# Kernel tuning notes

Measured on AMD Instinct MI355X. Metric: run time of the kernel, lower is better.

## Reference

```python
import jax, jax.numpy as jnp
import numpy as np

B, S, D, H = 4, 1024, 1024, 16
DH = D // H  # head_dim = 64


def setup_inputs() -> dict:
    key = jax.random.key(0)
    kq, kk, kv, kl, kwq, kwk, kwv, kwo = jax.random.split(key, 8)
    query = jax.random.normal(kq, (B, S, D), dtype=jnp.float32)
    key_t = jax.random.normal(kk, (B, S, D), dtype=jnp.float32)
    value = jax.random.normal(kv, (B, S, D), dtype=jnp.float32)
    # padding: keys at positions >= valid length are padded (True)
    lengths = jax.random.randint(kl, (B,), S // 2, S + 1)
    key_padding_mask = jnp.arange(S)[None, :] >= lengths[:, None]  # [B,S] bool
    scale = 1.0 / np.sqrt(D)
    Wq = jax.random.normal(kwq, (D, D), dtype=jnp.float32) * scale
    Wk = jax.random.normal(kwk, (D, D), dtype=jnp.float32) * scale
    Wv = jax.random.normal(kwv, (D, D), dtype=jnp.float32) * scale
    Wo = jax.random.normal(kwo, (D, D), dtype=jnp.float32) * scale
    gamma = jnp.ones((H,), dtype=jnp.float32)
    return {"query": query, "key": key_t, "value": value,
            "key_padding_mask": key_padding_mask,
            "Wq": Wq, "Wk": Wk, "Wv": Wv, "Wo": Wo, "gamma": gamma}


def reference(query, key, value, key_padding_mask, Wq, Wk, Wv, Wo, gamma):
    # nn.Linear(x) = x @ W.T (bias=False)
    q = jnp.einsum('bsd,ed->bse', query, Wq).reshape(B, S, H, DH).transpose(0, 2, 1, 3)  # [B,H,S,Dh]
    k = jnp.einsum('bsd,ed->bse', key, Wk).reshape(B, S, H, DH).transpose(0, 2, 1, 3)
    v = jnp.einsum('bsd,ed->bse', value, Wv).reshape(B, S, H, DH).transpose(0, 2, 1, 3)
    scores = jnp.einsum('bhqd,bhkd->bhqk', q, k) / jnp.sqrt(jnp.float32(DH))
    pad = key_padding_mask[:, None, None, :]  # [B,1,1,S]
    scores = jnp.where(pad, -jnp.inf, scores)
    v = jnp.where(key_padding_mask[:, None, :, None], 0.0, v)
    attn = jax.nn.softmax(scores, axis=-1)  # dropout p=0 (eval) -> identity
    ws = jnp.einsum('bhqk,bhkd->bhqd', attn, v)
    ws = ws * gamma[None, :, None, None]  # per-head scale
    ws = ws.transpose(0, 2, 1, 3).reshape(B, S, D)
    return jnp.einsum('bsd,ed->bse', ws, Wo)
```

## Files before the change

### kernel.cpp

```cpp
#include <hip/hip_runtime.h>
#include <math.h>

typedef __attribute__((ext_vector_type(8))) short bf16x8;
typedef __attribute__((ext_vector_type(4))) short bf16x4;
typedef __attribute__((ext_vector_type(4))) float f32x4;

#define MFMA16(a, b, c) __builtin_amdgcn_mfma_f32_16x16x32_bf16(a, b, c, 0, 0, 0)

#define WPL (1024u * 1024u)
#define XPL (4u * 1024u * 1024u)

__device__ __forceinline__ unsigned short rne_bf16(float f) {
    unsigned u = __float_as_uint(f);
    u += 0x7FFFu + ((u >> 16) & 1u);
    return (unsigned short)(u >> 16);
}

typedef const __attribute__((address_space(1))) unsigned int* gas_t;
typedef __attribute__((address_space(3))) unsigned int* las_t;
__device__ __forceinline__ void glds16(const void* g, void* l) {
    __builtin_amdgcn_global_load_lds((gas_t)g, (las_t)l, 16, 0, 0);
}

__global__ __launch_bounds__(256)
void convert_all(const float* __restrict__ Wq, const float* __restrict__ Wk,
                 const float* __restrict__ Wv, const float* __restrict__ Wo,
                 const float* __restrict__ Xq, const float* __restrict__ Xk,
                 const float* __restrict__ Xv,
                 unsigned short* __restrict__ Wb, unsigned short* __restrict__ Xb) {
    int blk = blockIdx.x;
    const float* S;
    unsigned short* D;
    if (blk < 4096) {
        int which = blk >> 10;
        S = which == 0 ? Wq : which == 1 ? Wk : which == 2 ? Wv : Wo;
        D = Wb + (size_t)which * WPL;
        blk &= 1023;
    } else {
        blk -= 4096;
        int which = blk >> 12;
        S = which == 0 ? Xq : which == 1 ? Xk : Xv;
        D = Xb + (size_t)which * XPL;
        blk &= 4095;
    }
    int i = (blk * 256 + threadIdx.x) * 4;
    float4 f = *(const float4*)&S[i];
    bf16x4 h;
    h[0] = (short)rne_bf16(f.x);
    h[1] = (short)rne_bf16(f.y);
    h[2] = (short)rne_bf16(f.z);
    h[3] = (short)rne_bf16(f.w);
    *(bf16x4*)&D[i] = h;
}

__global__ __launch_bounds__(256)
void gemm_ab(const unsigned short* __restrict__ Abase,
             const unsigned short* __restrict__ Bbase,
             unsigned short* __restrict__ QKV, float* __restrict__ Cf,
             int modeBase) {
    __shared__ unsigned short AS[128 * 64], BS[128 * 64];
    const int z = blockIdx.z, mode = modeBase + z;
    const unsigned short* A = Abase + (size_t)z * XPL;
    const unsigned short* B = Bbase + (size_t)z * WPL;

    const int t = threadIdx.x, lane = t & 63, w = t >> 6;
    const int quad = lane >> 4, l15 = lane & 15;
    const int wr = w & 1, wc = w >> 1;
    const int rowBase = blockIdx.y * 128, colBase = blockIdx.x * 128;

    const int srow = lane >> 3;
    const int cg = ((lane & 7) + 2 * srow) & 7;
    const unsigned short *gA[4], *gB[4];
    unsigned short *lA[4], *lB[4];
    #pragma unroll
    for (int e = 0; e < 4; e++) {
        int row = e * 32 + w * 8 + srow;
        gA[e] = A + (size_t)(rowBase + row) * 1024 + cg * 8;
        gB[e] = B + (size_t)(colBase + row) * 1024 + cg * 8;
        lA[e] = &AS[(e * 32 + w * 8) * 64];
        lB[e] = &BS[(e * 32 + w * 8) * 64];
    }

    const int s0 = (quad - 2 * l15) & 7;
    const int c0 = s0 * 8, c1 = ((s0 + 4) & 7) * 8;
    int aOff[4], bOff[4];
    #pragma unroll
    for (int i = 0; i < 4; i++) {
        aOff[i] = (wr * 64 + i * 16 + l15) * 64;
        bOff[i] = (wc * 64 + i * 16 + l15) * 64;
    }

    f32x4 acc[4][4] = {};

    for (int kt = 0; kt < 16; kt++) {
        if (kt) __syncthreads();
        const int ko = kt * 64;
        #pragma unroll
        for (int e = 0; e < 4; e++) {
            glds16(gA[e] + ko, lA[e]);
            glds16(gB[e] + ko, lB[e]);
        }
        __syncthreads();

        bf16x8 af[4], bfr[4];
        #pragma unroll
        for (int i = 0; i < 4; i++) af[i] = *(const bf16x8*)&AS[aOff[i] + c0];
        #pragma unroll
        for (int j = 0; j < 4; j++) bfr[j] = *(const bf16x8*)&BS[bOff[j] + c0];
        #pragma unroll
        for (int j = 0; j < 4; j++)
            #pragma unroll
            for (int i = 0; i < 4; i++)
                acc[i][j] = MFMA16(af[i], bfr[j], acc[i][j]);

        #pragma unroll
        for (int i = 0; i < 4; i++) af[i] = *(const bf16x8*)&AS[aOff[i] + c1];
        #pragma unroll
        for (int j = 0; j < 4; j++) bfr[j] = *(const bf16x8*)&BS[bOff[j] + c1];
        #pragma unroll
        for (int j = 0; j < 4; j++)
            #pragma unroll
            for (int i = 0; i < 4; i++)
                acc[i][j] = MFMA16(af[i], bfr[j], acc[i][j]);
    }

    if (mode == 3) {
        #pragma unroll
        for (int i = 0; i < 4; i++)
            #pragma unroll
            for (int j = 0; j < 4; j++)
                #pragma unroll
                for (int r = 0; r < 4; r++) {
                    int m = rowBase + wr * 64 + i * 16 + quad * 4 + r;
                    int n = colBase + wc * 64 + j * 16 + l15;
                    Cf[(size_t)m * 1024 + n] = acc[i][j][r];
                }
    } else {
        unsigned short* O = QKV + (size_t)z * XPL;
        #pragma unroll
        for (int i = 0; i < 4; i++)
            #pragma unroll
            for (int j = 0; j < 4; j++)
                #pragma unroll
                for (int r = 0; r < 4; r++) {
                    int m = rowBase + wr * 64 + i * 16 + quad * 4 + r;
                    int n = colBase + wc * 64 + j * 16 + l15;
                    int bb = m >> 10, s = m & 1023, hh = n >> 6, dh = n & 63;
                    size_t hb = ((size_t)(bb * 16 + hh)) << 16;
                    unsigned short v = rne_bf16(acc[i][j][r]);
                    if (mode == 0) {
                        O[hb + s * 64 + dh] = v;
                    } else if (mode == 1) {
                        O[hb + (size_t)((s >> 4) * 2 + (dh >> 5)) * 512 +
                          ((dh >> 3) & 3) * 128 + (s & 15) * 8 + (dh & 7)] = v;
                    } else {
                        O[hb + (size_t)((dh >> 4) * 32 + (s >> 5)) * 512 +
                          ((s >> 3) & 3) * 128 + (dh & 15) * 8 + (s & 7)] = v;
                    }
                }
    }
}

__global__ __launch_bounds__(256)
void attn_flat(const unsigned short* __restrict__ Qp,
               const unsigned short* __restrict__ Kf,
               const unsigned short* __restrict__ Vf,
               const int* __restrict__ mask, const float* __restrict__ gamma,
               unsigned short* __restrict__ WSr) {
    __shared__ int maskS[1024];
    __shared__ unsigned short Ph[4][32 * 72];

    const int t = threadIdx.x, lane = t & 63, w = t >> 6;
    const int quad = lane >> 4, l15 = lane & 15;
    const int q0 = blockIdx.x * 128, h = blockIdx.y, b = blockIdx.z;
    const size_t hb = ((size_t)(b * 16 + h)) << 16;

    ((int4*)maskS)[t] = ((const int4*)(mask + b * 1024))[t];

    bf16x8 qf[2][2];
    #pragma unroll
    for (int mi = 0; mi < 2; mi++) {
        size_t qb = hb + (size_t)(q0 + w * 32 + mi * 16 + l15) * 64 + quad * 8;
        qf[mi][0] = *(const bf16x8*)&Qp[qb];
        qf[mi][1] = *(const bf16x8*)&Qp[qb + 32];
    }

    f32x4 o[2][4] = {};
    float lsum[2][4] = {{0.f, 0.f, 0.f, 0.f}, {0.f, 0.f, 0.f, 0.f}};
    unsigned short* P = Ph[w];

    __syncthreads();

    for (int jt = 0; jt < 16; jt++) {
        const int j0 = jt * 64;
        if (maskS[j0]) break;
        const bool partial = maskS[j0 + 63] != 0;

        bf16x8 kv[4][2];
        #pragma unroll
        for (int nj = 0; nj < 4; nj++)
            #pragma unroll
            for (int kk = 0; kk < 2; kk++)
                kv[nj][kk] = *(const bf16x8*)&Kf[hb + (size_t)((jt * 4 + nj) * 2 + kk) * 512 + lane * 8];

        f32x4 s4[2][4] = {};
        #pragma unroll
        for (int nj = 0; nj < 4; nj++)
            #pragma unroll
            for (int kk = 0; kk < 2; kk++)
                #pragma unroll
                for (int mi = 0; mi < 2; mi++)
                    s4[mi][nj] = MFMA16(qf[mi][kk], kv[nj][kk], s4[mi][nj]);

        bf16x8 vv[4][2];
        #pragma unroll
        for (int dt = 0; dt < 4; dt++)
            #pragma unroll
            for (int ks = 0; ks < 2; ks++)
                vv[dt][ks] = *(const bf16x8*)&Vf[hb + (size_t)(dt * 32 + jt * 2 + ks) * 512 + lane * 8];

        #pragma unroll
        for (int mi = 0; mi < 2; mi++)
            #pragma unroll
            for (int nj = 0; nj < 4; nj++) {
                int mk = partial ? maskS[j0 + nj * 16 + l15] : 0;
                #pragma unroll
                for (int r = 0; r < 4; r++) {
                    float p = mk ? 0.f : __expf(s4[mi][nj][r] * 0.125f);
                    lsum[mi][r] += p;
                    int rowW = mi * 16 + quad * 4 + r;
                    int slot = ((nj * 2 + (l15 >> 3)) - 2 * rowW) & 7;
                    P[rowW * 72 + slot * 8 + (l15 & 7)] = rne_bf16(p);
                }
            }

        bf16x8 pf[2][2];
        #pragma unroll
        for (int mi = 0; mi < 2; mi++) {
            int rowR = mi * 16 + l15;
            int sl0 = (quad - 2 * rowR) & 7;
            pf[mi][0] = *(const bf16x8*)&P[rowR * 72 + sl0 * 8];
            pf[mi][1] = *(const bf16x8*)&P[rowR * 72 + ((sl0 + 4) & 7) * 8];
        }
        #pragma unroll
        for (int dt = 0; dt < 4; dt++)
            #pragma unroll
            for (int ks = 0; ks < 2; ks++)
                #pragma unroll
                for (int mi = 0; mi < 2; mi++)
                    o[mi][dt] = MFMA16(pf[mi][ks], vv[dt][ks], o[mi][dt]);
    }

    #pragma unroll
    for (int mi = 0; mi < 2; mi++)
        #pragma unroll
        for (int r = 0; r < 4; r++) {
            lsum[mi][r] += __shfl_xor(lsum[mi][r], 1);
            lsum[mi][r] += __shfl_xor(lsum[mi][r], 2);
            lsum[mi][r] += __shfl_xor(lsum[mi][r], 4);
            lsum[mi][r] += __shfl_xor(lsum[mi][r], 8);
        }

    const float g = gamma[h];
    #pragma unroll
    for (int mi = 0; mi < 2; mi++)
        #pragma unroll
        for (int r = 0; r < 4; r++) {
            int qrow = q0 + w * 32 + mi * 16 + quad * 4 + r;
            float sc = g / lsum[mi][r];
            size_t base = ((size_t)b * 1024 + qrow) * 1024 + h * 64;
            #pragma unroll
            for (int dt = 0; dt < 4; dt++)
                WSr[base + dt * 16 + l15] = rne_bf16(o[mi][dt][r] * sc);
        }
}

extern "C" void kernel_launch(void* const* d_in, const int* in_sizes, int n_in,
                              void* d_out, int out_size, void* d_ws, size_t ws_size,
                              hipStream_t stream) {
    const float* query = (const float*)d_in[0];
    const float* key   = (const float*)d_in[1];
    const float* value = (const float*)d_in[2];
    const int*   mask  = (const int*)d_in[3];
    const float* Wq    = (const float*)d_in[4];
    const float* Wk    = (const float*)d_in[5];
    const float* Wv    = (const float*)d_in[6];
    const float* Wo    = (const float*)d_in[7];
    const float* gamma = (const float*)d_in[8];
    float* out = (float*)d_out;

    unsigned short* u = (unsigned short*)d_ws;
    unsigned short* Xb  = u;
    unsigned short* QKV = u + 3 * XPL;
    unsigned short* Wb  = u + 6 * XPL;
    unsigned short* WSr = Xb;
    unsigned short* Qp = QKV, *Kfp = QKV + XPL, *Vfp = QKV + 2 * XPL;
    unsigned short* Wob = Wb + 3 * WPL;

    convert_all<<<16384, 256, 0, stream>>>(Wq, Wk, Wv, Wo, query, key, value, Wb, Xb);

    gemm_ab<<<dim3(8, 32, 3), 256, 0, stream>>>(Xb, Wb, QKV, nullptr, 0);

    attn_flat<<<dim3(8, 16, 4), 256, 0, stream>>>(Qp, Kfp, Vfp, mask, gamma, WSr);

    gemm_ab<<<dim3(8, 32, 1), 256, 0, stream>>>(WSr, Wob, nullptr, out, 3);
}
```

Before: 217.1 us.

## Double-buffer LDS tiles in GEMM to prefetch next K-slice during MFMA

Splits the shared-memory A/B tiles into two buffers. The next K tile is issued via global_load_lds into the alternate buffer before computing on the current one, with a single barrier per iteration. The aim is to overlap global-to-LDS transfer latency with MFMA compute. In exchange, LDS use per block doubles, which may lower occupancy, and correctness relies on the barrier waiting for outstanding async LDS loads.

```diff
diff --git a/kernel.cpp b/kernel.cpp
--- a/kernel.cpp
+++ b/kernel.cpp
@@ -58,7 +58,7 @@
              const unsigned short* __restrict__ Bbase,
              unsigned short* __restrict__ QKV, float* __restrict__ Cf,
              int modeBase) {
-    __shared__ unsigned short AS[128 * 64], BS[128 * 64];
+    __shared__ unsigned short AS[2][128 * 64], BS[2][128 * 64];
     const int z = blockIdx.z, mode = modeBase + z;
     const unsigned short* A = Abase + (size_t)z * XPL;
     const unsigned short* B = Bbase + (size_t)z * WPL;
@@ -71,14 +71,13 @@
     const int srow = lane >> 3;
     const int cg = ((lane & 7) + 2 * srow) & 7;
     const unsigned short *gA[4], *gB[4];
-    unsigned short *lA[4], *lB[4];
+    int lOff[4];
     #pragma unroll
     for (int e = 0; e < 4; e++) {
         int row = e * 32 + w * 8 + srow;
         gA[e] = A + (size_t)(rowBase + row) * 1024 + cg * 8;
         gB[e] = B + (size_t)(colBase + row) * 1024 + cg * 8;
-        lA[e] = &AS[(e * 32 + w * 8) * 64];
-        lB[e] = &BS[(e * 32 + w * 8) * 64];
+        lOff[e] = (e * 32 + w * 8) * 64;
     }
 
     const int s0 = (quad - 2 * l15) & 7;
@@ -92,21 +91,29 @@
 
     f32x4 acc[4][4] = {};
 
+    #pragma unroll
+    for (int e = 0; e < 4; e++) {
+        glds16(gA[e], &AS[0][lOff[e]]);
+        glds16(gB[e], &BS[0][lOff[e]]);
+    }
+    __syncthreads();
+
     for (int kt = 0; kt < 16; kt++) {
-        if (kt) __syncthreads();
-        const int ko = kt * 64;
-        #pragma unroll
-        for (int e = 0; e < 4; e++) {
-            glds16(gA[e] + ko, lA[e]);
-            glds16(gB[e] + ko, lB[e]);
+        const int buf = kt & 1;
+        if (kt + 1 < 16) {
+            const int ko = (kt + 1) * 64, nb = buf ^ 1;
+            #pragma unroll
+            for (int e = 0; e < 4; e++) {
+                glds16(gA[e] + ko, &AS[nb][lOff[e]]);
+                glds16(gB[e] + ko, &BS[nb][lOff[e]]);
+            }
         }
-        __syncthreads();
 
         bf16x8 af[4], bfr[4];
         #pragma unroll
-        for (int i = 0; i < 4; i++) af[i] = *(const bf16x8*)&AS[aOff[i] + c0];
-        #pragma unroll
-        for (int j = 0; j < 4; j++) bfr[j] = *(const bf16x8*)&BS[bOff[j] + c0];
+        for (int i = 0; i < 4; i++) af[i] = *(const bf16x8*)&AS[buf][aOff[i] + c0];
+        #pragma unroll
+        for (int j = 0; j < 4; j++) bfr[j] = *(const bf16x8*)&BS[buf][bOff[j] + c0];
         #pragma unroll
         for (int j = 0; j < 4; j++)
             #pragma unroll
@@ -114,14 +121,16 @@
                 acc[i][j] = MFMA16(af[i], bfr[j], acc[i][j]);
 
         #pragma unroll
-        for (int i = 0; i < 4; i++) af[i] = *(const bf16x8*)&AS[aOff[i] + c1];
-        #pragma unroll
-        for (int j = 0; j < 4; j++) bfr[j] = *(const bf16x8*)&BS[bOff[j] + c1];
+        for (int i = 0; i < 4; i++) af[i] = *(const bf16x8*)&AS[buf][aOff[i] + c1];
+        #pragma unroll
+        for (int j = 0; j < 4; j++) bfr[j] = *(const bf16x8*)&BS[buf][bOff[j] + c1];
         #pragma unroll
         for (int j = 0; j < 4; j++)
             #pragma unroll
             for (int i = 0; i < 4; i++)
                 acc[i][j] = MFMA16(af[i], bfr[j], acc[i][j]);
+
+        __syncthreads();
     }
 
     if (mode == 3) {
```

Measured after the change: 222.2 us. 1.02x slower.

## Split GEMM kernel, use BK=32 XOR-swizzled tiles and narrower output-projection tiles

Applied to the files above, without the earlier changes.

Replaces the shared mode-switched GEMM with two specialised kernels. The K tile shrinks from 64 to 32, which halves LDS use per block, and the shared-memory layout switches to an XOR swizzle. The output projection now uses 128x64 tiles, doubling its grid from 256 to 512 blocks so more CUs are busy. The cost is twice as many K iterations, each with its own barriers, and less MFMA work between syncs.

```diff
diff --git a/kernel.cpp b/kernel.cpp
--- a/kernel.cpp
+++ b/kernel.cpp
@@ -54,111 +54,165 @@
 }
 
 __global__ __launch_bounds__(256)
-void gemm_ab(const unsigned short* __restrict__ Abase,
-             const unsigned short* __restrict__ Bbase,
-             unsigned short* __restrict__ QKV, float* __restrict__ Cf,
-             int modeBase) {
-    __shared__ unsigned short AS[128 * 64], BS[128 * 64];
-    const int z = blockIdx.z, mode = modeBase + z;
-    const unsigned short* A = Abase + (size_t)z * XPL;
-    const unsigned short* B = Bbase + (size_t)z * WPL;
+void gemm_proj(const unsigned short* __restrict__ Xbase,
+               const unsigned short* __restrict__ Wb,
+               unsigned short* __restrict__ QKV) {
+    __shared__ unsigned short AS[128 * 32];
+    __shared__ unsigned short BS[128 * 32];
+
+    const int z = blockIdx.z;
+    const unsigned short* A = Xbase + (size_t)z * XPL;
+    const unsigned short* B = Wb + (size_t)z * WPL;
 
     const int t = threadIdx.x, lane = t & 63, w = t >> 6;
     const int quad = lane >> 4, l15 = lane & 15;
     const int wr = w & 1, wc = w >> 1;
     const int rowBase = blockIdx.y * 128, colBase = blockIdx.x * 128;
 
-    const int srow = lane >> 3;
-    const int cg = ((lane & 7) + 2 * srow) & 7;
-    const unsigned short *gA[4], *gB[4];
-    unsigned short *lA[4], *lB[4];
-    #pragma unroll
-    for (int e = 0; e < 4; e++) {
-        int row = e * 32 + w * 8 + srow;
+    const unsigned short* gA[2];
+    const unsigned short* gB[2];
+    unsigned short* lA[2];
+    unsigned short* lB[2];
+    #pragma unroll
+    for (int e = 0; e < 2; e++) {
+        int row = w * 32 + e * 16 + (lane >> 2);
+        int cg = (lane & 3) ^ ((row >> 1) & 3);
         gA[e] = A + (size_t)(rowBase + row) * 1024 + cg * 8;
         gB[e] = B + (size_t)(colBase + row) * 1024 + cg * 8;
-        lA[e] = &AS[(e * 32 + w * 8) * 64];
-        lB[e] = &BS[(e * 32 + w * 8) * 64];
-    }
-
-    const int s0 = (quad - 2 * l15) & 7;
-    const int c0 = s0 * 8, c1 = ((s0 + 4) & 7) * 8;
-    int aOff[4], bOff[4];
+        lA[e] = &AS[(w * 32 + e * 16) * 32];
+        lB[e] = &BS[(w * 32 + e * 16) * 32];
+    }
+
+    int aAd[4], bAd[4];
     #pragma unroll
     for (int i = 0; i < 4; i++) {
-        aOff[i] = (wr * 64 + i * 16 + l15) * 64;
-        bOff[i] = (wc * 64 + i * 16 + l15) * 64;
+        int ra = wr * 64 + i * 16 + l15;
+        aAd[i] = ra * 32 + (quad ^ ((ra >> 1) & 3)) * 8;
+        int rb = wc * 64 + i * 16 + l15;
+        bAd[i] = rb * 32 + (quad ^ ((rb >> 1) & 3)) * 8;
     }
 
     f32x4 acc[4][4] = {};
 
-    for (int kt = 0; kt < 16; kt++) {
+    for (int kt = 0; kt < 32; kt++) {
         if (kt) __syncthreads();
-        const int ko = kt * 64;
-        #pragma unroll
-        for (int e = 0; e < 4; e++) {
-            glds16(gA[e] + ko, lA[e]);
-            glds16(gB[e] + ko, lB[e]);
-        }
+        const int ko = kt * 32;
+        glds16(gA[0] + ko, lA[0]);
+        glds16(gA[1] + ko, lA[1]);
+        glds16(gB[0] + ko, lB[0]);
+        glds16(gB[1] + ko, lB[1]);
         __syncthreads();
 
         bf16x8 af[4], bfr[4];
         #pragma unroll
-        for (int i = 0; i < 4; i++) af[i] = *(const bf16x8*)&AS[aOff[i] + c0];
-        #pragma unroll
-        for (int j = 0; j < 4; j++) bfr[j] = *(const bf16x8*)&BS[bOff[j] + c0];
+        for (int i = 0; i < 4; i++) af[i] = *(const bf16x8*)&AS[aAd[i]];
+        #pragma unroll
+        for (int j = 0; j < 4; j++) bfr[j] = *(const bf16x8*)&BS[bAd[j]];
         #pragma unroll
         for (int j = 0; j < 4; j++)
             #pragma unroll
             for (int i = 0; i < 4; i++)
                 acc[i][j] = MFMA16(af[i], bfr[j], acc[i][j]);
-
-        #pragma unroll
-        for (int i = 0; i < 4; i++) af[i] = *(const bf16x8*)&AS[aOff[i] + c1];
-        #pragma unroll
-        for (int j = 0; j < 4; j++) bfr[j] = *(const bf16x8*)&BS[bOff[j] + c1];
+    }
+
+    unsigned short* O = QKV + (size_t)z * XPL;
+    #pragma unroll
+    for (int i = 0; i < 4; i++)
         #pragma unroll
         for (int j = 0; j < 4; j++)
             #pragma unroll
+            for (int r = 0; r < 4; r++) {
+                int m = rowBase + wr * 64 + i * 16 + quad * 4 + r;
+                int n = colBase + wc * 64 + j * 16 + l15;
+                int bb = m >> 10, s = m & 1023, hh = n >> 6, dh = n & 63;
+                size_t hb = ((size_t)(bb * 16 + hh)) << 16;
+                unsigned short v = rne_bf16(acc[i][j][r]);
+                if (z == 0) {
+                    O[hb + s * 64 + dh] = v;
+                } else if (z == 1) {
+                    O[hb + (size_t)((s >> 4) * 2 + (dh >> 5)) * 512 +
+                      ((dh >> 3) & 3) * 128 + (s & 15) * 8 + (dh & 7)] = v;
+                } else {
+                    O[hb + (size_t)((dh >> 4) * 32 + (s >> 5)) * 512 +
+                      ((s >> 3) & 3) * 128 + (dh & 15) * 8 + (s & 7)] = v;
+                }
+            }
+}
+
+__global__ __launch_bounds__(256)
+void gemm_out1(const unsigned short* __restrict__ A,
+               const unsigned short* __restrict__ Bh,
+               float* __restrict__ Cf) {
+    __shared__ unsigned short AS[128 * 32];
+    __shared__ unsigned short BhS[64 * 32];
+
+    const int t = threadIdx.x, lane = t & 63, w = t >> 6;
+    const int quad = lane >> 4, l15 = lane & 15;
+    const int wr = w & 1, wc = w >> 1;
+    const int rowBase = blockIdx.y * 128, colBase = blockIdx.x * 64;
+
+    const unsigned short* gA[2];
+    unsigned short* lA[2];
+    #pragma unroll
+    for (int e = 0; e < 2; e++) {
+        int row = w * 32 + e * 16 + (lane >> 2);
+        int cg = (lane & 3) ^ ((row >> 1) & 3);
+        gA[e] = A + (size_t)(rowBase + row) * 1024 + cg * 8;
+        lA[e] = &AS[(w * 32 + e * 16) * 32];
+    }
+    const unsigned short* gBh;
+    unsigned short* lBh;
+    {
+        int row = w * 16 + (lane >> 2);
+        int cg = (lane & 3) ^ ((row >> 1) & 3);
+        gBh = Bh + (size_t)(colBase + row) * 1024 + cg * 8;
+        lBh = &BhS[(w * 16) * 32];
+    }
+
+    int aAd[4], bAd[2];
+    #pragma unroll
+    for (int i = 0; i < 4; i++) {
+        int ra = wr * 64 + i * 16 + l15;
+        aAd[i] = ra * 32 + (quad ^ ((ra >> 1) & 3)) * 8;
+    }
+    #pragma unroll
+    for (int j = 0; j < 2; j++) {
+        int rb = wc * 32 + j * 16 + l15;
+        bAd[j] = rb * 32 + (quad ^ ((rb >> 1) & 3)) * 8;
+    }
+
+    f32x4 acc[4][2] = {};
+
+    for (int kt = 0; kt < 32; kt++) {
+        if (kt) __syncthreads();
+        const int ko = kt * 32;
+        glds16(gA[0] + ko, lA[0]);
+        glds16(gA[1] + ko, lA[1]);
+        glds16(gBh + ko, lBh);
+        __syncthreads();
+
+        bf16x8 af[4], bhf[2];
+        #pragma unroll
+        for (int i = 0; i < 4; i++) af[i] = *(const bf16x8*)&AS[aAd[i]];
+        #pragma unroll
+        for (int j = 0; j < 2; j++) bhf[j] = *(const bf16x8*)&BhS[bAd[j]];
+        #pragma unroll
+        for (int j = 0; j < 2; j++)
+            #pragma unroll
             for (int i = 0; i < 4; i++)
-                acc[i][j] = MFMA16(af[i], bfr[j], acc[i][j]);
-    }
-
-    if (mode == 3) {
-        #pragma unroll
-        for (int i = 0; i < 4; i++)
-            #pragma unroll
-            for (int j = 0; j < 4; j++)
-                #pragma unroll
-                for (int r = 0; r < 4; r++) {
-                    int m = rowBase + wr * 64 + i * 16 + quad * 4 + r;
-                    int n = colBase + wc * 64 + j * 16 + l15;
-                    Cf[(size_t)m * 1024 + n] = acc[i][j][r];
-                }
-    } else {
-        unsigned short* O = QKV + (size_t)z * XPL;
-        #pragma unroll
-        for (int i = 0; i < 4; i++)
-            #pragma unroll
-            for (int j = 0; j < 4; j++)
-                #pragma unroll
-                for (int r = 0; r < 4; r++) {
-                    int m = rowBase + wr * 64 + i * 16 + quad * 4 + r;
-                    int n = colBase + wc * 64 + j * 16 + l15;
-                    int bb = m >> 10, s = m & 1023, hh = n >> 6, dh = n & 63;
-                    size_t hb = ((size_t)(bb * 16 + hh)) << 16;
-                    unsigned short v = rne_bf16(acc[i][j][r]);
-                    if (mode == 0) {
-                        O[hb + s * 64 + dh] = v;
-                    } else if (mode == 1) {
-                        O[hb + (size_t)((s >> 4) * 2 + (dh >> 5)) * 512 +
-                          ((dh >> 3) & 3) * 128 + (s & 15) * 8 + (dh & 7)] = v;
-                    } else {
-                        O[hb + (size_t)((dh >> 4) * 32 + (s >> 5)) * 512 +
-                          ((s >> 3) & 3) * 128 + (dh & 15) * 8 + (s & 7)] = v;
-                    }
-                }
-    }
+                acc[i][j] = MFMA16(af[i], bhf[j], acc[i][j]);
+    }
+
+    #pragma unroll
+    for (int i = 0; i < 4; i++)
+        #pragma unroll
+        for (int j = 0; j < 2; j++)
+            #pragma unroll
+            for (int r = 0; r < 4; r++) {
+                int m = rowBase + wr * 64 + i * 16 + quad * 4 + r;
+                int n = colBase + wc * 32 + j * 16 + l15;
+                Cf[(size_t)m * 1024 + n] = acc[i][j][r];
+            }
 }
 
 __global__ __launch_bounds__(256)
@@ -299,9 +353,9 @@
 
     convert_all<<<16384, 256, 0, stream>>>(Wq, Wk, Wv, Wo, query, key, value, Wb, Xb);
 
-    gemm_ab<<<dim3(8, 32, 3), 256, 0, stream>>>(Xb, Wb, QKV, nullptr, 0);
+    gemm_proj<<<dim3(8, 32, 3), 256, 0, stream>>>(Xb, Wb, QKV);
 
     attn_flat<<<dim3(8, 16, 4), 256, 0, stream>>>(Qp, Kfp, Vfp, mask, gamma, WSr);
 
-    gemm_ab<<<dim3(8, 32, 1), 256, 0, stream>>>(WSr, Wob, nullptr, out, 3);
-}
+    gemm_out1<<<dim3(16, 32), 256, 0, stream>>>(WSr, Wob, out);
+}
```

After: 219.0 us. Within noise of the previous version (+0.9%).
